# Performance work log

Measured on AMD Instinct MI355X. Metric: run time of the kernel, lower is better.

The kernel has to match this reference:

```python
import jax, jax.numpy as jnp
import numpy as np

N_HEADS = 16
ROPE_THETA = 10000.0


def _rope_tables(seq_len, head_dim, dtype=jnp.float32):
    half = head_dim // 2
    inv_freq = 1.0 / (ROPE_THETA ** (jnp.arange(0, half, dtype=jnp.float32) / half))
    t = jnp.arange(seq_len, dtype=jnp.float32)
    freqs = jnp.outer(t, inv_freq)  # (S, half)
    return jnp.cos(freqs).astype(dtype), jnp.sin(freqs).astype(dtype)


def _apply_rope(x, cos, sin):
    # x: (B, H, S, hd); cos/sin: (S, hd//2)
    half = x.shape[-1] // 2
    x1, x2 = x[..., :half], x[..., half:]
    c = cos[None, None, :, :]
    s = sin[None, None, :, :]
    return jnp.concatenate([x1 * c - x2 * s, x1 * s + x2 * c], axis=-1)


def setup_inputs() -> dict:
    key = jax.random.key(0)
    k1, k2, k3 = jax.random.split(key, 3)
    B, S, D = 4, 2048, 2048
    hd = D // N_HEADS
    x = jax.random.normal(k1, (B, S, D), dtype=jnp.float32)
    cos, sin = _rope_tables(S, hd)
    w_qkv = jax.random.normal(k2, (D, 3 * D), dtype=jnp.float32) * (D ** -0.5)
    w_out = jax.random.normal(k3, (D, D), dtype=jnp.float32) * (D ** -0.5)
    return {"x": x, "cos": cos, "sin": sin, "w_qkv": w_qkv, "w_out": w_out}


def reference(x, cos, sin, w_qkv, w_out):
    B, S, D = x.shape
    H = N_HEADS
    hd = D // H
    qkv = x @ w_qkv  # (B, S, 3D)
    qkv = qkv.reshape(B, S, 3, H, hd).transpose(2, 0, 3, 1, 4)  # (3, B, H, S, hd)
    q, k, v = qkv[0], qkv[1], qkv[2]
    q = _apply_rope(q, cos, sin)
    k = _apply_rope(k, cos, sin)
    scale = 1.0 / jnp.sqrt(jnp.asarray(hd, dtype=x.dtype))
    scores = jnp.einsum('bhqd,bhkd->bhqk', q, k) * scale  # (B, H, S, S)
    causal = jnp.tril(jnp.ones((S, S), dtype=bool))
    scores = jnp.where(causal[None, None, :, :], scores, jnp.asarray(-1e30, dtype=scores.dtype))
    p = jax.nn.softmax(scores, axis=-1)
    out = jnp.einsum('bhqk,bhkd->bhqd', p, v)  # (B, H, S, hd)
    out = out.transpose(0, 2, 1, 3).reshape(B, S, D)
    return out @ w_out
```

## Files before the change

kernel.cpp:

```cpp
#include <hip/hip_runtime.h>
#include <hip/hip_bf16.h>
#include <stdint.h>

typedef __bf16  bf16x8  __attribute__((ext_vector_type(8)));
typedef float   floatx4 __attribute__((ext_vector_type(4)));

typedef __attribute__((address_space(1))) void gvoid_t;
typedef __attribute__((address_space(3))) void svoid_t;

__device__ __forceinline__ void gld16(ushort* lds, const ushort* g) {
  __builtin_amdgcn_global_load_lds((gvoid_t*)g, (svoid_t*)lds, 16, 0, 0);
}

__device__ __forceinline__ ushort f2bf(float f) {
  union { float f; unsigned u; } v; v.f = f;
  unsigned u = v.u;
  return (ushort)((u + 0x7fffu + ((u >> 16) & 1u)) >> 16);
}
__device__ __forceinline__ float bf2f(ushort h) {
  union { unsigned u; float f; } v; v.u = ((unsigned)h) << 16; return v.f;
}
__device__ __forceinline__ unsigned pk2bf(float a, float b) {
  __hip_bfloat162 h = __float22bfloat162_rn(make_float2(a, b));
  union { __hip_bfloat162 h; unsigned u; } v; v.h = h; return v.u;
}

__global__ __launch_bounds__(256) void cvt_f32_bf16(
    const float* __restrict__ in, ushort* __restrict__ out) {
  int i = blockIdx.x * 256 + threadIdx.x;
  float4 a = ((const float4*)in)[i];
  ushort4 o;
  o.x = f2bf(a.x); o.y = f2bf(a.y); o.z = f2bf(a.z); o.w = f2bf(a.w);
  ((ushort4*)out)[i] = o;
}

__global__ __launch_bounds__(256) void transpose_cvt(
    const float* __restrict__ in, ushort* __restrict__ out, int R, int C) {
  __shared__ ushort tile[64][65];
  const int r0 = blockIdx.y * 64, c0 = blockIdx.x * 64;
  const int t = threadIdx.x;
#pragma unroll
  for (int rep = 0; rep < 16; rep++) {
    int idx = rep * 256 + t;
    int r = idx >> 6, c = idx & 63;
    tile[r][c] = f2bf(in[(size_t)(r0 + r) * C + c0 + c]);
  }
  __syncthreads();
#pragma unroll
  for (int rep = 0; rep < 16; rep++) {
    int idx = rep * 256 + t;
    int r = idx >> 6, c = idx & 63;
    out[(size_t)(c0 + r) * R + r0 + c] = tile[c][r];
  }
}

template <int EPI>
__global__ __launch_bounds__(256) void gemm128(
    const ushort* __restrict__ A, const ushort* __restrict__ Bt,
    float* __restrict__ Cf,
    ushort* __restrict__ C0, ushort* __restrict__ C1, ushort* __restrict__ C2,
    int M, int N, int K) {
  __shared__ __align__(16) ushort As[128 * 64];
  __shared__ __align__(16) ushort Bs[128 * 64];
  const int t = threadIdx.x;
  const int lane = t & 63;
  const int w = t >> 6;
  const int l15 = lane & 15;
  const int quad = lane >> 4;
  const int m0 = blockIdx.y * 128;
  const int n0 = blockIdx.x * 128;
  const int wm = (w >> 1) * 64;
  const int wn = (w & 1) * 64;

  floatx4 acc[4][4];
  const floatx4 zero = {0.f, 0.f, 0.f, 0.f};
#pragma unroll
  for (int i = 0; i < 4; i++)
#pragma unroll
    for (int j = 0; j < 4; j++) acc[i][j] = zero;

  for (int kb = 0; kb < K; kb += 64) {
    __syncthreads();
#pragma unroll
    for (int it = 0; it < 4; it++) {
      int o = (w * 4 + it) * 64 + lane;
      int row = o >> 3;
      int c = (o & 7) ^ (row & 7);
      gld16(&As[(w * 4 + it) * 512], A + (size_t)(m0 + row) * K + kb + c * 8);
      gld16(&Bs[(w * 4 + it) * 512], Bt + (size_t)(n0 + row) * K + kb + c * 8);
    }
    __syncthreads();
#pragma unroll
    for (int kk = 0; kk < 2; kk++) {
      bf16x8 af[4], bf[4];
#pragma unroll
      for (int i = 0; i < 4; i++) {
        int row = wm + i * 16 + l15;
        int c = (kk * 4 + quad) ^ (row & 7);
        af[i] = *(const bf16x8*)&As[row * 64 + c * 8];
      }
#pragma unroll
      for (int j = 0; j < 4; j++) {
        int row = wn + j * 16 + l15;
        int c = (kk * 4 + quad) ^ (row & 7);
        bf[j] = *(const bf16x8*)&Bs[row * 64 + c * 8];
      }
#pragma unroll
      for (int i = 0; i < 4; i++)
#pragma unroll
        for (int j = 0; j < 4; j++)
          acc[i][j] = __builtin_amdgcn_mfma_f32_16x16x32_bf16(af[i], bf[j],
                                                              acc[i][j], 0, 0, 0);
    }
  }

  if (EPI == 0) {
#pragma unroll
    for (int i = 0; i < 4; i++)
#pragma unroll
      for (int j = 0; j < 4; j++)
#pragma unroll
        for (int r = 0; r < 4; r++) {
          int m = m0 + wm + i * 16 + quad * 4 + r;
          int n = n0 + wn + j * 16 + l15;
          Cf[(size_t)m * N + n] = acc[i][j][r];
        }
  } else {
    const int qkvsel = n0 >> 11;
    const int h = (n0 >> 7) & 15;
#pragma unroll
    for (int i = 0; i < 4; i++)
#pragma unroll
      for (int j = 0; j < 4; j++) {
        int d = wn + j * 16 + l15;
        if (qkvsel < 2) {
          ushort* dst = (qkvsel == 0) ? C0 : C1;
#pragma unroll
          for (int r = 0; r < 4; r++) {
            int m = m0 + wm + i * 16 + quad * 4 + r;
            int b = m >> 11, s = m & 2047;
            dst[((size_t)(b * 16 + h) * 2048 + s) * 128 + d] = f2bf(acc[i][j][r]);
          }
        } else {
          int m = m0 + wm + i * 16 + quad * 4;
          int b = m >> 11, s = m & 2047;
          ushort4 pk;
          pk.x = f2bf(acc[i][j][0]);
          pk.y = f2bf(acc[i][j][1]);
          pk.z = f2bf(acc[i][j][2]);
          pk.w = f2bf(acc[i][j][3]);
          *(ushort4*)&C2[((size_t)(b * 16 + h) * 128 + d) * 2048 + s] = pk;
        }
      }
  }
}

__global__ __launch_bounds__(256) void rope_kernel(
    ushort* __restrict__ Q, ushort* __restrict__ Kb,
    const float* __restrict__ cosT, const float* __restrict__ sinT) {
  unsigned gid = blockIdx.x * 256u + threadIdx.x;
  int d = gid & 63;
  int s = (gid >> 6) & 2047;
  int bh = (gid >> 17) & 63;
  const bool isK = (gid >> 23) != 0;
  ushort* buf = isK ? Kb : Q;
  const float sc = isK ? 1.0f
                       : 0.08838834764831845f * 1.4426950408889634f;
  size_t base = ((size_t)bh * 2048 + s) * 128;
  float x1 = bf2f(buf[base + d]);
  float x2 = bf2f(buf[base + d + 64]);
  float c = cosT[s * 64 + d];
  float sn = sinT[s * 64 + d];
  buf[base + d] = f2bf((x1 * c - x2 * sn) * sc);
  buf[base + d + 64] = f2bf((x1 * sn + x2 * c) * sc);
}

__global__ __launch_bounds__(256, 4) void attn_kernel(
    const ushort* __restrict__ Q, const ushort* __restrict__ Kb,
    const ushort* __restrict__ VT, ushort* __restrict__ O) {
  __shared__ __align__(16) ushort Ks[64 * 128];
  __shared__ __align__(16) ushort Vs[128 * 64];
  __shared__ __align__(16) ushort Ps[64 * 64];
  const int t = threadIdx.x, lane = t & 63, w = t >> 6;
  const int l15 = lane & 15, quad = lane >> 4;
  const int bid = blockIdx.x;
  const int tq = 31 - (bid >> 6);
  const int bh = bid & 63;
  const int q0 = tq * 64 + w * 16;
  const int qrow = q0 + l15;
  const size_t hbase = (size_t)bh * 2048 * 128;
  const float NEGINF = -__builtin_inff();

  bf16x8 aq[4];
#pragma unroll
  for (int kb = 0; kb < 4; kb++)
    aq[kb] = *(const bf16x8*)&Q[hbase + (size_t)qrow * 128 + kb * 32 + quad * 8];

  float m2 = NEGINF, lsum = 0.f;
  floatx4 oacc[8];
  const floatx4 zero = {0.f, 0.f, 0.f, 0.f};
#pragma unroll
  for (int dj = 0; dj < 8; dj++) oacc[dj] = zero;

  const int ntk = tq + 1;

  for (int tk = 0; tk < ntk; tk++) {
    __syncthreads();
#pragma unroll
    for (int it = 0; it < 4; it++) {
      int o = (w * 4 + it) * 64 + lane;
      {
        int row = o >> 4;
        int c = (o & 15) ^ (row & 15);
        gld16(&Ks[(w * 4 + it) * 512],
              Kb + hbase + (size_t)(tk * 64 + row) * 128 + c * 8);
      }
      {
        int row = o >> 3;
        int c = (o & 7) ^ (row & 7);
        gld16(&Vs[(w * 4 + it) * 512],
              VT + hbase + (size_t)row * 2048 + tk * 64 + c * 8);
      }
    }
    __syncthreads();

    floatx4 sacc[4];
#pragma unroll
    for (int j = 0; j < 4; j++) sacc[j] = zero;
#pragma unroll
    for (int kb = 0; kb < 4; kb++) {
#pragma unroll
      for (int j = 0; j < 4; j++) {
        int row = j * 16 + l15;
        int c = (kb * 4 + quad) ^ (row & 15);
        bf16x8 kf = *(const bf16x8*)&Ks[row * 128 + c * 8];
        sacc[j] = __builtin_amdgcn_mfma_f32_16x16x32_bf16(kf, aq[kb], sacc[j],
                                                          0, 0, 0);
      }
    }

    if (tk == tq) {
#pragma unroll
      for (int j = 0; j < 4; j++)
#pragma unroll
        for (int r = 0; r < 4; r++) {
          int kcol = tk * 64 + j * 16 + quad * 4 + r;
          if (kcol > qrow) sacc[j][r] = NEGINF;
        }
    }

    float mx = sacc[0][0];
#pragma unroll
    for (int j = 0; j < 4; j++)
#pragma unroll
      for (int r = 0; r < 4; r++) mx = fmaxf(mx, sacc[j][r]);
    mx = fmaxf(mx, __shfl_xor(mx, 16));
    mx = fmaxf(mx, __shfl_xor(mx, 32));
    float mnew = fmaxf(m2, mx);
    float alpha = __builtin_exp2f(m2 - mnew);
    m2 = mnew;
    float rs = 0.f;
#pragma unroll
    for (int j = 0; j < 4; j++)
#pragma unroll
      for (int r = 0; r < 4; r++) {
        float p = __builtin_exp2f(sacc[j][r] - mnew);
        sacc[j][r] = p;
        rs += p;
      }
    rs += __shfl_xor(rs, 16);
    rs += __shfl_xor(rs, 32);
    lsum = lsum * alpha + rs;
    if (__any(alpha < 1.0f)) {
#pragma unroll
      for (int dj = 0; dj < 8; dj++) oacc[dj] *= alpha;
    }

#pragma unroll
    for (int j = 0; j < 4; j++) {
      unsigned lo = pk2bf(sacc[j][0], sacc[j][1]);
      unsigned hi = pk2bf(sacc[j][2], sacc[j][3]);
      int g = j * 2 + (quad >> 1);
      int gp = g ^ (l15 & 7);
      uint2 pv; pv.x = lo; pv.y = hi;
      *(uint2*)&Ps[(w * 16 + l15) * 64 + gp * 8 + (quad & 1) * 4] = pv;
    }

    bf16x8 bp[2];
#pragma unroll
    for (int kk = 0; kk < 2; kk++) {
      int g = kk * 4 + quad;
      int gp = g ^ (l15 & 7);
      bp[kk] = *(const bf16x8*)&Ps[(w * 16 + l15) * 64 + gp * 8];
    }
#pragma unroll
    for (int kk = 0; kk < 2; kk++)
#pragma unroll
      for (int dj = 0; dj < 8; dj++) {
        int rowd = dj * 16 + l15;
        int c = (kk * 4 + quad) ^ (rowd & 7);
        bf16x8 av = *(const bf16x8*)&Vs[rowd * 64 + c * 8];
        oacc[dj] = __builtin_amdgcn_mfma_f32_16x16x32_bf16(av, bp[kk], oacc[dj],
                                                           0, 0, 0);
      }
  }

  const int b = bh >> 4, h = bh & 15;
  const float rl = 1.0f / lsum;
  const size_t obase = ((size_t)(b * 2048 + qrow)) * 2048 + h * 128;
#pragma unroll
  for (int dj = 0; dj < 8; dj++) {
    ushort4 pk;
    pk.x = f2bf(oacc[dj][0] * rl);
    pk.y = f2bf(oacc[dj][1] * rl);
    pk.z = f2bf(oacc[dj][2] * rl);
    pk.w = f2bf(oacc[dj][3] * rl);
    *(ushort4*)&O[obase + dj * 16 + quad * 4] = pk;
  }
}

extern "C" void kernel_launch(void* const* d_in, const int* in_sizes, int n_in,
                              void* d_out, int out_size, void* d_ws, size_t ws_size,
                              hipStream_t stream) {
  const float* x    = (const float*)d_in[0];
  const float* cosT = (const float*)d_in[1];
  const float* sinT = (const float*)d_in[2];
  const float* wqkv = (const float*)d_in[3];
  const float* wout = (const float*)d_in[4];
  float* out = (float*)d_out;
  char* ws = (char*)d_ws;

  ushort* xbf   = (ushort*)d_out;
  ushort* wqkvT = (ushort*)(ws);
  ushort* Ob    = (ushort*)(ws);
  ushort* woutT = (ushort*)(ws + 33554432);
  ushort* Qb    = (ushort*)(ws + 41943040);
  ushort* Kbuf  = (ushort*)(ws + 75497472);
  ushort* VTb   = (ushort*)(ws + 109051904);

  cvt_f32_bf16<<<16384, 256, 0, stream>>>(x, xbf);
  transpose_cvt<<<dim3(96, 32), 256, 0, stream>>>(wqkv, wqkvT, 2048, 6144);
  transpose_cvt<<<dim3(32, 32), 256, 0, stream>>>(wout, woutT, 2048, 2048);
  gemm128<1><<<dim3(48, 64), 256, 0, stream>>>(xbf, wqkvT, nullptr,
                                               Qb, Kbuf, VTb, 8192, 6144, 2048);
  rope_kernel<<<65536, 256, 0, stream>>>(Qb, Kbuf, cosT, sinT);
  attn_kernel<<<2048, 256, 0, stream>>>(Qb, Kbuf, VTb, Ob);
  gemm128<0><<<dim3(16, 64), 256, 0, stream>>>(Ob, woutT, out,
                                               nullptr, nullptr, nullptr,
                                               8192, 2048, 2048);
}
```

Baseline: 629.7 us.

## Enlarge GEMM tiles to 256x256 with double-buffered LDS prefetch pipeline

Replaces the 128x128 single-buffered GEMM with a 256x256 tile kernel using 512 threads and double-buffered LDS. Global-to-LDS loads for the next K-step are spread across the compute sub-phases, with explicit waitcnt, barriers and MFMA priority raising. The intent is to hide memory latency behind MFMA work and raise arithmetic intensity per block. The cost is 128KB of LDS per block and fewer blocks: one block per CU, and the output projection runs only 256 blocks, which risks poor occupancy and tail effects.

```diff
diff --git a/kernel.cpp b/kernel.cpp
--- a/kernel.cpp
+++ b/kernel.cpp
@@ -55,103 +55,160 @@
 }
 
 template <int EPI>
-__global__ __launch_bounds__(256) void gemm128(
+__global__ __launch_bounds__(512, 2) void gemm256(
     const ushort* __restrict__ A, const ushort* __restrict__ Bt,
     float* __restrict__ Cf,
     ushort* __restrict__ C0, ushort* __restrict__ C1, ushort* __restrict__ C2,
     int M, int N, int K) {
-  __shared__ __align__(16) ushort As[128 * 64];
-  __shared__ __align__(16) ushort Bs[128 * 64];
+  __shared__ __align__(16) ushort As[2][256 * 64];
+  __shared__ __align__(16) ushort Bs[2][256 * 64];
   const int t = threadIdx.x;
   const int lane = t & 63;
   const int w = t >> 6;
   const int l15 = lane & 15;
   const int quad = lane >> 4;
-  const int m0 = blockIdx.y * 128;
-  const int n0 = blockIdx.x * 128;
-  const int wm = (w >> 1) * 64;
-  const int wn = (w & 1) * 64;
-
-  floatx4 acc[4][4];
+  const int m0 = blockIdx.y * 256;
+  const int n0 = blockIdx.x * 256;
+  const int wmB = (w >> 2) * 128;
+  const int wnB = (w & 3) * 64;
+
+  const int srow = t >> 3;
+  const int sc = (t & 7) ^ (srow & 7);
+  const ushort* pA = A + (size_t)(m0 + srow) * K + sc * 8;
+  const ushort* pB = Bt + (size_t)(n0 + srow) * K + sc * 8;
+  const size_t rstep = (size_t)64 * K;
+
+  floatx4 acc[8][4];
   const floatx4 zero = {0.f, 0.f, 0.f, 0.f};
 #pragma unroll
-  for (int i = 0; i < 4; i++)
+  for (int i = 0; i < 8; i++)
 #pragma unroll
     for (int j = 0; j < 4; j++) acc[i][j] = zero;
 
-  for (int kb = 0; kb < K; kb += 64) {
-    __syncthreads();
-#pragma unroll
-    for (int it = 0; it < 4; it++) {
-      int o = (w * 4 + it) * 64 + lane;
-      int row = o >> 3;
-      int c = (o & 7) ^ (row & 7);
-      gld16(&As[(w * 4 + it) * 512], A + (size_t)(m0 + row) * K + kb + c * 8);
-      gld16(&Bs[(w * 4 + it) * 512], Bt + (size_t)(n0 + row) * K + kb + c * 8);
-    }
-    __syncthreads();
-#pragma unroll
-    for (int kk = 0; kk < 2; kk++) {
-      bf16x8 af[4], bf[4];
-#pragma unroll
-      for (int i = 0; i < 4; i++) {
-        int row = wm + i * 16 + l15;
-        int c = (kk * 4 + quad) ^ (row & 7);
-        af[i] = *(const bf16x8*)&As[row * 64 + c * 8];
-      }
-#pragma unroll
-      for (int j = 0; j < 4; j++) {
-        int row = wn + j * 16 + l15;
-        int c = (kk * 4 + quad) ^ (row & 7);
-        bf[j] = *(const bf16x8*)&Bs[row * 64 + c * 8];
-      }
-#pragma unroll
-      for (int i = 0; i < 4; i++)
-#pragma unroll
-        for (int j = 0; j < 4; j++)
-          acc[i][j] = __builtin_amdgcn_mfma_f32_16x16x32_bf16(af[i], bf[j],
-                                                              acc[i][j], 0, 0, 0);
+  const int NT = K >> 6;
+
+#pragma unroll
+  for (int it = 0; it < 4; ++it)
+    gld16(&As[0][(it * 512 + w * 64) * 8], pA + it * rstep);
+#pragma unroll
+  for (int it = 0; it < 4; ++it)
+    gld16(&Bs[0][(it * 512 + w * 64) * 8], pB + it * rstep);
+
+  for (int kt = 0; kt < NT; ++kt) {
+    const int cb = kt & 1;
+    const ushort* cA = As[cb];
+    const ushort* cB = Bs[cb];
+    ushort* nA = As[cb ^ 1];
+    ushort* nB = Bs[cb ^ 1];
+    const int kb2 = (kt + 1) << 6;
+    const bool pf = (kt + 1 < NT);
+
+    if (pf) {
+      gld16(&nA[(0 * 512 + w * 64) * 8], pA + 0 * rstep + kb2);
+      gld16(&nA[(1 * 512 + w * 64) * 8], pA + 1 * rstep + kb2);
+      asm volatile("s_waitcnt vmcnt(2)" ::: "memory");
+    } else {
+      asm volatile("s_waitcnt vmcnt(0)" ::: "memory");
+    }
+    __builtin_amdgcn_s_barrier();
+
+    bf16x8 bf[4];
+#pragma unroll
+    for (int kk = 0; kk < 2; ++kk) {
+#pragma unroll
+      for (int mh = 0; mh < 2; ++mh) {
+        bf16x8 af[4];
+#pragma unroll
+        for (int m = 0; m < 4; ++m) {
+          int row = wmB + (mh * 4 + m) * 16 + l15;
+          int c = (kk * 4 + quad) ^ (row & 7);
+          af[m] = *(const bf16x8*)&cA[row * 64 + c * 8];
+        }
+        if (mh == 0) {
+#pragma unroll
+          for (int n = 0; n < 4; ++n) {
+            int row = wnB + n * 16 + l15;
+            int c = (kk * 4 + quad) ^ (row & 7);
+            bf[n] = *(const bf16x8*)&cB[row * 64 + c * 8];
+          }
+        }
+        if (pf) {
+          const int p = kk * 2 + mh;
+          if (p == 0) {
+            gld16(&nA[(2 * 512 + w * 64) * 8], pA + 2 * rstep + kb2);
+            gld16(&nA[(3 * 512 + w * 64) * 8], pA + 3 * rstep + kb2);
+          } else if (p == 1) {
+            gld16(&nB[(0 * 512 + w * 64) * 8], pB + 0 * rstep + kb2);
+            gld16(&nB[(1 * 512 + w * 64) * 8], pB + 1 * rstep + kb2);
+          } else if (p == 2) {
+            gld16(&nB[(2 * 512 + w * 64) * 8], pB + 2 * rstep + kb2);
+            gld16(&nB[(3 * 512 + w * 64) * 8], pB + 3 * rstep + kb2);
+          }
+        }
+        __builtin_amdgcn_s_barrier();
+        asm volatile("s_waitcnt lgkmcnt(0)" ::: "memory");
+        __builtin_amdgcn_sched_barrier(0);
+        __builtin_amdgcn_s_setprio(1);
+#pragma unroll
+        for (int m = 0; m < 4; ++m)
+#pragma unroll
+          for (int n = 0; n < 4; ++n)
+            acc[mh * 4 + m][n] = __builtin_amdgcn_mfma_f32_16x16x32_bf16(
+                af[m], bf[n], acc[mh * 4 + m][n], 0, 0, 0);
+        __builtin_amdgcn_s_setprio(0);
+        __builtin_amdgcn_sched_barrier(0);
+        __builtin_amdgcn_s_barrier();
+      }
     }
   }
 
   if (EPI == 0) {
 #pragma unroll
-    for (int i = 0; i < 4; i++)
-#pragma unroll
-      for (int j = 0; j < 4; j++)
-#pragma unroll
-        for (int r = 0; r < 4; r++) {
-          int m = m0 + wm + i * 16 + quad * 4 + r;
-          int n = n0 + wn + j * 16 + l15;
-          Cf[(size_t)m * N + n] = acc[i][j][r];
+    for (int m = 0; m < 8; ++m)
+#pragma unroll
+      for (int n = 0; n < 4; ++n)
+#pragma unroll
+        for (int r = 0; r < 4; ++r) {
+          int row = m0 + wmB + m * 16 + quad * 4 + r;
+          int col = n0 + wnB + n * 16 + l15;
+          Cf[(size_t)row * N + col] = acc[m][n][r];
         }
   } else {
-    const int qkvsel = n0 >> 11;
-    const int h = (n0 >> 7) & 15;
-#pragma unroll
-    for (int i = 0; i < 4; i++)
-#pragma unroll
-      for (int j = 0; j < 4; j++) {
-        int d = wn + j * 16 + l15;
-        if (qkvsel < 2) {
-          ushort* dst = (qkvsel == 0) ? C0 : C1;
-#pragma unroll
-          for (int r = 0; r < 4; r++) {
-            int m = m0 + wm + i * 16 + quad * 4 + r;
-            int b = m >> 11, s = m & 2047;
-            dst[((size_t)(b * 16 + h) * 2048 + s) * 128 + d] = f2bf(acc[i][j][r]);
-          }
-        } else {
-          int m = m0 + wm + i * 16 + quad * 4;
-          int b = m >> 11, s = m & 2047;
+    const int colW = n0 + wnB;
+    const int sel = colW >> 11;
+    const int h = (colW >> 7) & 15;
+    if (sel < 2) {
+      ushort* dst = (sel == 0) ? C0 : C1;
+#pragma unroll
+      for (int m = 0; m < 8; ++m) {
+        int rowb = m0 + wmB + m * 16 + quad * 4;
+        int b = rowb >> 11, s = rowb & 2047;
+#pragma unroll
+        for (int n = 0; n < 4; ++n) {
+          int d = (colW + n * 16 + l15) & 127;
+#pragma unroll
+          for (int r = 0; r < 4; ++r)
+            dst[((size_t)(b * 16 + h) * 2048 + (s + r)) * 128 + d] =
+                f2bf(acc[m][n][r]);
+        }
+      }
+    } else {
+#pragma unroll
+      for (int m = 0; m < 8; ++m) {
+        int rowb = m0 + wmB + m * 16 + quad * 4;
+        int b = rowb >> 11, s = rowb & 2047;
+#pragma unroll
+        for (int n = 0; n < 4; ++n) {
+          int d = (colW + n * 16 + l15) & 127;
           ushort4 pk;
-          pk.x = f2bf(acc[i][j][0]);
-          pk.y = f2bf(acc[i][j][1]);
-          pk.z = f2bf(acc[i][j][2]);
-          pk.w = f2bf(acc[i][j][3]);
+          pk.x = f2bf(acc[m][n][0]);
+          pk.y = f2bf(acc[m][n][1]);
+          pk.z = f2bf(acc[m][n][2]);
+          pk.w = f2bf(acc[m][n][3]);
           *(ushort4*)&C2[((size_t)(b * 16 + h) * 128 + d) * 2048 + s] = pk;
         }
       }
+    }
   }
 }
 
@@ -341,11 +398,11 @@
   cvt_f32_bf16<<<16384, 256, 0, stream>>>(x, xbf);
   transpose_cvt<<<dim3(96, 32), 256, 0, stream>>>(wqkv, wqkvT, 2048, 6144);
   transpose_cvt<<<dim3(32, 32), 256, 0, stream>>>(wout, woutT, 2048, 2048);
-  gemm128<1><<<dim3(48, 64), 256, 0, stream>>>(xbf, wqkvT, nullptr,
+  gemm256<1><<<dim3(24, 32), 512, 0, stream>>>(xbf, wqkvT, nullptr,
                                                Qb, Kbuf, VTb, 8192, 6144, 2048);
   rope_kernel<<<65536, 256, 0, stream>>>(Qb, Kbuf, cosT, sinT);
   attn_kernel<<<2048, 256, 0, stream>>>(Qb, Kbuf, VTb, Ob);
-  gemm128<0><<<dim3(16, 64), 256, 0, stream>>>(Ob, woutT, out,
-                                               nullptr, nullptr, nullptr,
-                                               8192, 2048, 2048);
-}
+  gemm256<0><<<dim3(8, 32), 512, 0, stream>>>(Ob, woutT, out,
+                                              nullptr, nullptr, nullptr,
+                                              8192, 2048, 2048);
+}
```

New measurement: 606.7 us. -3.7%, faster.
